# Performance work log

Hardware: AMD Instinct MI355X
Metric: run time of the kernel (lower is better)

Reference implementation:

```python
import jax, jax.numpy as jnp
import numpy as np

HEADS = 16
LN_EPS = 1e-5


def setup_inputs() -> dict:
    key = jax.random.key(0)
    ks = jax.random.split(key, 8)
    B, S, D = 2, 2048, 1024
    F = 4 * D
    std = 0.02
    return {
        "x": jax.random.normal(ks[0], (B, S, D), jnp.float32),
        # QKV projections (stored as (in, out)); kaiming-normal-like scale
        "Wq": jax.random.normal(ks[1], (D, D), jnp.float32) * std,
        "bq": jnp.zeros((D,), jnp.float32),
        "Wk": jax.random.normal(ks[2], (D, D), jnp.float32) * std,
        "bk": jnp.zeros((D,), jnp.float32),
        "Wv": jax.random.normal(ks[3], (D, D), jnp.float32) * std,
        "bv": jnp.zeros((D,), jnp.float32),
        # FFN
        "W1": jax.random.normal(ks[4], (D, F), jnp.float32) * std,
        "b1": jnp.zeros((F,), jnp.float32),
        "W2": jax.random.normal(ks[5], (F, D), jnp.float32) * std,
        "b2": jnp.zeros((D,), jnp.float32),
        # LayerNorm
        "gamma": jnp.ones((D,), jnp.float32),
        "beta": jnp.zeros((D,), jnp.float32),
    }


def reference(x, Wq, bq, Wk, bk, Wv, bv, W1, b1, W2, b2, gamma, beta):
    B, S, D = x.shape
    H = HEADS
    hd = D // H
    # QKV projections -> [B, H, S, hd]
    Q = (x @ Wq + bq).reshape(B, S, H, hd).transpose(0, 2, 1, 3)
    K = (x @ Wk + bk).reshape(B, S, H, hd).transpose(0, 2, 1, 3)
    V = (x @ Wv + bv).reshape(B, S, H, hd).transpose(0, 2, 1, 3)
    # scores scaled by sqrt(embedding_dim), faithful to source (not head_dim)
    scores = jnp.einsum('bhqd,bhkd->bhqk', Q, K) / jnp.sqrt(jnp.asarray(D, x.dtype))
    attn = jax.nn.softmax(scores, axis=-1)
    # diagonal_training: zero the diagonal of the post-softmax attention matrix
    attn = attn * (1.0 - jnp.eye(S, dtype=attn.dtype))
    out = jnp.einsum('bhqk,bhkd->bhqd', attn, V)
    out = out.transpose(0, 2, 1, 3).reshape(B, S, D)
    # dropout is identity in eval mode
    h = jax.nn.gelu(out @ W1 + b1, approximate=False) @ W2 + b2
    # LayerNorm
    mu = jnp.mean(h, axis=-1, keepdims=True)
    var = jnp.var(h, axis=-1, keepdims=True)
    return (h - mu) * jax.lax.rsqrt(var + LN_EPS) * gamma + beta
```

## Files before the change

kernel.cpp:

```cpp
#include <hip/hip_runtime.h>

using bf16x8 = __attribute__((ext_vector_type(8))) short;
using f32x4  = __attribute__((ext_vector_type(4))) float;

__device__ __forceinline__ float b2f(ushort u) {
  union { unsigned int i; float f; } v; v.i = ((unsigned int)u) << 16; return v.f;
}
__device__ __forceinline__ ushort f2b(float f) {
  unsigned int x = __float_as_uint(f);
  unsigned int r = (x + 0x7FFFu + ((x >> 16) & 1u)) >> 16;
  return (ushort)r;
}

__device__ __forceinline__ void gld_lds16(const void* g, void* l) {
  __builtin_amdgcn_global_load_lds(
      (const __attribute__((address_space(1))) void*)g,
      (__attribute__((address_space(3))) void*)l, 16, 0, 0);
}


__global__ void cast_bf16_kernel(const float* __restrict__ in, ushort* __restrict__ out, int n) {
  int i = (blockIdx.x * blockDim.x + threadIdx.x) * 4;
  if (i < n) {
    float4 v = *(const float4*)(in + i);
    ushort4 o = make_ushort4(f2b(v.x), f2b(v.y), f2b(v.z), f2b(v.w));
    *(ushort4*)(out + i) = o;
  }
}

__global__ void transpose_cast_kernel(const float* __restrict__ in, ushort* __restrict__ out,
                                      int R, int C) {
  __shared__ float tile[32][33];
  int tx = threadIdx.x, ty = threadIdx.y;
  int cb = blockIdx.x * 32, rb = blockIdx.y * 32;
  for (int i = ty; i < 32; i += 8)
    tile[i][tx] = in[(size_t)(rb + i) * C + (cb + tx)];
  __syncthreads();
  for (int i = ty; i < 32; i += 8)
    out[(size_t)(cb + i) * R + (rb + tx)] = f2b(tile[tx][i]);
}

__global__ void transpose_v_kernel(const ushort* __restrict__ V, ushort* __restrict__ Vt) {
  __shared__ ushort t[32][33];
  int bh = blockIdx.z;
  int s0 = blockIdx.x * 32, d0 = blockIdx.y * 32;
  const ushort* Vb = V + (size_t)bh * 2048 * 64;
  ushort* Vtb = Vt + (size_t)bh * 64 * 2048;
  int tx = threadIdx.x, ty = threadIdx.y;
  for (int i = ty; i < 32; i += 8) t[i][tx] = Vb[(size_t)(s0 + i) * 64 + d0 + tx];
  __syncthreads();
  for (int i = ty; i < 32; i += 8) Vtb[(size_t)(d0 + i) * 2048 + s0 + tx] = t[tx][i];
}


#define BM 128
#define BN 128
#define BK 32

template<int EPI>
__global__ __launch_bounds__(256) void gemm_bf16(
    const ushort* __restrict__ A, const ushort* __restrict__ Bt,
    const float* __restrict__ bias, void* __restrict__ Cout, void* __restrict__ Cout2,
    int M, int N, int Kstride, int k_len)
{
  __shared__ ushort Asm_[2][BM * BK];
  __shared__ ushort Bsm_[2][BN * BK];
  const int bm = blockIdx.x * BM, bn = blockIdx.y * BN;
  const int k_begin = blockIdx.z * k_len;
  const int tid = threadIdx.x;
  const int lane = tid & 63, w = tid >> 6;
  const int wm = (w >> 1) * 64, wn = (w & 1) * 64;
  const int g = lane >> 4, c = lane & 15;
  const int srow = tid >> 2, scol = (tid & 3) * 8;
  const int soff = srow * 32 + scol;

  const ushort* gA0 = A  + (size_t)(bm + srow) * Kstride + k_begin + scol;
  const ushort* gA1 = gA0 + (size_t)64 * Kstride;
  const ushort* gB0 = Bt + (size_t)(bn + srow) * Kstride + k_begin + scol;
  const ushort* gB1 = gB0 + (size_t)64 * Kstride;

  f32x4 acc[4][4] = {};
  const int nt = k_len / BK;

  gld_lds16(gA0, &Asm_[0][soff]);
  gld_lds16(gA1, &Asm_[0][64 * 32 + soff]);
  gld_lds16(gB0, &Bsm_[0][soff]);
  gld_lds16(gB1, &Bsm_[0][64 * 32 + soff]);
  __syncthreads();

  int cur = 0;
  for (int t = 0; t < nt; ++t) {
    if (t + 1 < nt) {
      int k0 = (t + 1) * BK;
      gld_lds16(gA0 + k0, &Asm_[cur ^ 1][soff]);
      gld_lds16(gA1 + k0, &Asm_[cur ^ 1][64 * 32 + soff]);
      gld_lds16(gB0 + k0, &Bsm_[cur ^ 1][soff]);
      gld_lds16(gB1 + k0, &Bsm_[cur ^ 1][64 * 32 + soff]);
    }
    bf16x8 af[4], bfr[4];
    #pragma unroll
    for (int m = 0; m < 4; ++m)
      af[m] = *(const bf16x8*)&Asm_[cur][(wm + m * 16 + c) * 32 + g * 8];
    #pragma unroll
    for (int n = 0; n < 4; ++n)
      bfr[n] = *(const bf16x8*)&Bsm_[cur][(wn + n * 16 + c) * 32 + g * 8];
    #pragma unroll
    for (int m = 0; m < 4; ++m)
      #pragma unroll
      for (int n = 0; n < 4; ++n)
        acc[m][n] = __builtin_amdgcn_mfma_f32_16x16x32_bf16(af[m], bfr[n], acc[m][n], 0, 0, 0);
    __syncthreads();
    cur ^= 1;
  }

  #pragma unroll
  for (int n = 0; n < 4; ++n) {
    int col = bn + wn + n * 16 + c;
    float bia = bias ? bias[col] : 0.0f;
    #pragma unroll
    for (int m = 0; m < 4; ++m) {
      #pragma unroll
      for (int r = 0; r < 4; ++r) {
        int row = bm + wm + m * 16 + g * 4 + r;
        float v = acc[m][n][r] + bia;
        if (EPI == 1) {
          float u = 0.7978845608028654f * (v + 0.044715f * v * v * v);
          float au = fabsf(u);
          float e = __expf(-2.0f * au);
          float th = (1.0f - e) / (1.0f + e);
          th = copysignf(th, u);
          v = 0.5f * v * (1.0f + th);
        }
        if (EPI == 2) {
          float* dst = (blockIdx.z == 0) ? (float*)Cout : (float*)Cout2;
          dst[(size_t)row * N + col] = v;
        } else if (EPI == 3) {
          int b = row >> 11, s = row & 2047;
          int which = col >> 10, cc = col & 1023;
          int hh = cc >> 6, d = cc & 63;
          ((ushort*)Cout)[(size_t)which * 4194304 +
                          ((size_t)((b * 16 + hh) * 2048 + s)) * 64 + d] = f2b(v);
        } else {
          ((ushort*)Cout)[(size_t)row * N + col] = f2b(v);
        }
      }
    }
  }
}


#define ATT_SC 0.03125f

__global__ __launch_bounds__(256) void attn_kernel(
    const ushort* __restrict__ Q, const ushort* __restrict__ K,
    const ushort* __restrict__ V, const ushort* __restrict__ Vt,
    ushort* __restrict__ Out)
{
  const int bh = blockIdx.y;
  const int b = bh >> 4, h = bh & 15;
  const int q0 = blockIdx.x * 64;
  const int tid = threadIdx.x;
  const int w = tid >> 6, lane = tid & 63;
  const int hi = lane >> 4, c = lane & 15;
  const int qw = q0 + w * 16;

  const ushort* Qb = Q + (size_t)bh * 2048 * 64;
  const ushort* Kb = K + (size_t)bh * 2048 * 64;
  const ushort* Vb = V + (size_t)bh * 2048 * 64;
  const ushort* Vtb = Vt + (size_t)bh * 64 * 2048;

  __shared__ ushort Ksm[64 * 72];
  __shared__ ushort Vsm[64 * 72];
  __shared__ ushort Psm[4][16 * 72];

  bf16x8 qf0 = *(const bf16x8*)(Qb + (size_t)(qw + c) * 64 + hi * 8);
  bf16x8 qf1 = *(const bf16x8*)(Qb + (size_t)(qw + c) * 64 + 32 + hi * 8);

  f32x4 acc[4] = {};
  float m_run = -1e30f, l_run = 0.f;

  const int srow = tid >> 2;
  const int scol = (tid & 3) * 8;

  for (int j0 = 0; j0 < 2048; j0 += 64) {
    __syncthreads();
    *(int4*)&Ksm[srow * 72 + scol]      = *(const int4*)(Kb + (size_t)(j0 + srow) * 64 + scol);
    *(int4*)&Ksm[srow * 72 + 32 + scol] = *(const int4*)(Kb + (size_t)(j0 + srow) * 64 + 32 + scol);
    *(int4*)&Vsm[srow * 72 + scol]      = *(const int4*)(Vtb + (size_t)srow * 2048 + j0 + scol);
    *(int4*)&Vsm[srow * 72 + 32 + scol] = *(const int4*)(Vtb + (size_t)srow * 2048 + j0 + 32 + scol);
    __syncthreads();

    f32x4 sv[4];
    #pragma unroll
    for (int sub = 0; sub < 4; ++sub) {
      bf16x8 k0 = *(const bf16x8*)&Ksm[(sub * 16 + c) * 72 + hi * 8];
      bf16x8 k1 = *(const bf16x8*)&Ksm[(sub * 16 + c) * 72 + 32 + hi * 8];
      f32x4 z = {};
      z = __builtin_amdgcn_mfma_f32_16x16x32_bf16(k0, qf0, z, 0, 0, 0);
      z = __builtin_amdgcn_mfma_f32_16x16x32_bf16(k1, qf1, z, 0, 0, 0);
      #pragma unroll
      for (int r = 0; r < 4; ++r) sv[sub][r] = z[r] * ATT_SC;
    }

    float tm = -1e30f;
    #pragma unroll
    for (int sub = 0; sub < 4; ++sub)
      #pragma unroll
      for (int r = 0; r < 4; ++r) tm = fmaxf(tm, sv[sub][r]);
    tm = fmaxf(tm, __shfl_xor(tm, 16));
    tm = fmaxf(tm, __shfl_xor(tm, 32));
    float mnew = fmaxf(m_run, tm);
    float p[16];
    float psum = 0.f;
    #pragma unroll
    for (int sub = 0; sub < 4; ++sub)
      #pragma unroll
      for (int r = 0; r < 4; ++r) { float e = __expf(sv[sub][r] - mnew); p[sub * 4 + r] = e; psum += e; }
    psum += __shfl_xor(psum, 16);
    psum += __shfl_xor(psum, 32);
    float f = __expf(m_run - mnew);
    l_run = l_run * f + psum;
    m_run = mnew;

    #pragma unroll
    for (int r = 0; r < 4; ++r) {
      float fr = __shfl(f, hi * 4 + r, 16);
      #pragma unroll
      for (int dsub = 0; dsub < 4; ++dsub) acc[dsub][r] *= fr;
    }

    #pragma unroll
    for (int sub = 0; sub < 4; ++sub) {
      ushort4 pk = make_ushort4(f2b(p[sub * 4 + 0]), f2b(p[sub * 4 + 1]),
                                f2b(p[sub * 4 + 2]), f2b(p[sub * 4 + 3]));
      *(ushort4*)&Psm[w][c * 72 + sub * 16 + hi * 4] = pk;
    }
    asm volatile("" ::: "memory");

    bf16x8 pa0 = *(const bf16x8*)&Psm[w][c * 72 + hi * 8];
    bf16x8 pa1 = *(const bf16x8*)&Psm[w][c * 72 + 32 + hi * 8];
    #pragma unroll
    for (int dsub = 0; dsub < 4; ++dsub) {
      bf16x8 v0 = *(const bf16x8*)&Vsm[(dsub * 16 + c) * 72 + hi * 8];
      bf16x8 v1 = *(const bf16x8*)&Vsm[(dsub * 16 + c) * 72 + 32 + hi * 8];
      acc[dsub] = __builtin_amdgcn_mfma_f32_16x16x32_bf16(pa0, v0, acc[dsub], 0, 0, 0);
      acc[dsub] = __builtin_amdgcn_mfma_f32_16x16x32_bf16(pa1, v1, acc[dsub], 0, 0, 0);
    }
  }

  #pragma unroll
  for (int r = 0; r < 4; ++r) {
    int q = qw + hi * 4 + r;
    float part = 0.f;
    #pragma unroll
    for (int t = 0; t < 4; ++t)
      part += b2f(Qb[(size_t)q * 64 + c * 4 + t]) * b2f(Kb[(size_t)q * 64 + c * 4 + t]);
    #pragma unroll
    for (int off = 1; off < 16; off <<= 1) part += __shfl_xor(part, off);
    float mq = __shfl(m_run, hi * 4 + r, 16);
    float lq = __shfl(l_run, hi * 4 + r, 16);
    float pqq = __expf(part * ATT_SC - mq);
    float inv = 1.f / lq;
    #pragma unroll
    for (int dsub = 0; dsub < 4; ++dsub) {
      float vq = b2f(Vb[(size_t)q * 64 + dsub * 16 + c]);
      float o = (acc[dsub][r] - pqq * vq) * inv;
      Out[((size_t)(b * 2048 + q) * 16 + h) * 64 + dsub * 16 + c] = f2b(o);
    }
  }
}


__global__ __launch_bounds__(256) void ln_kernel(float* __restrict__ h,
                                                 const float* __restrict__ p1,
                                                 const float* __restrict__ b2,
                                                 const float* __restrict__ gamma,
                                                 const float* __restrict__ beta) {
  int row = blockIdx.x, tid = threadIdx.x;
  float* hr = h + (size_t)row * 1024;
  const float* pr = p1 + (size_t)row * 1024;
  float4 v = ((const float4*)hr)[tid];
  float4 p = ((const float4*)pr)[tid];
  float4 bb = ((const float4*)b2)[tid];
  v.x += p.x + bb.x; v.y += p.y + bb.y; v.z += p.z + bb.z; v.w += p.w + bb.w;
  float s = v.x + v.y + v.z + v.w;
  #pragma unroll
  for (int off = 1; off < 64; off <<= 1) s += __shfl_xor(s, off);
  __shared__ float red[2][4];
  int wv = tid >> 6, lane = tid & 63;
  if (lane == 0) red[0][wv] = s;
  __syncthreads();
  float mu = (red[0][0] + red[0][1] + red[0][2] + red[0][3]) * (1.0f / 1024.0f);
  float dx = v.x - mu, dy = v.y - mu, dz = v.z - mu, dw = v.w - mu;
  float q = dx * dx + dy * dy + dz * dz + dw * dw;
  #pragma unroll
  for (int off = 1; off < 64; off <<= 1) q += __shfl_xor(q, off);
  if (lane == 0) red[1][wv] = q;
  __syncthreads();
  float var = (red[1][0] + red[1][1] + red[1][2] + red[1][3]) * (1.0f / 1024.0f);
  float is = rsqrtf(var + 1e-5f);
  float4 gm = ((const float4*)gamma)[tid];
  float4 bt = ((const float4*)beta)[tid];
  float4 o;
  o.x = dx * is * gm.x + bt.x;
  o.y = dy * is * gm.y + bt.y;
  o.z = dz * is * gm.z + bt.z;
  o.w = dw * is * gm.w + bt.w;
  ((float4*)hr)[tid] = o;
}


extern "C" void kernel_launch(void* const* d_in, const int* in_sizes, int n_in,
                              void* d_out, int out_size, void* d_ws, size_t ws_size,
                              hipStream_t stream) {
  const float* x  = (const float*)d_in[0];
  const float* Wq = (const float*)d_in[1];
  const float* bq = (const float*)d_in[2];
  const float* Wk = (const float*)d_in[3];
  const float* bk = (const float*)d_in[4];
  const float* Wv = (const float*)d_in[5];
  const float* bv = (const float*)d_in[6];
  const float* W1 = (const float*)d_in[7];
  const float* b1 = (const float*)d_in[8];
  const float* W2 = (const float*)d_in[9];
  const float* b2 = (const float*)d_in[10];
  const float* gamma = (const float*)d_in[11];
  const float* beta  = (const float*)d_in[12];
  float* out = (float*)d_out;

  char* ws = (char*)d_ws;
  const size_t MB = 1u << 20;
  ushort* xb    = (ushort*)(ws + 0);
  ushort* Wqkvt = (ushort*)(ws + 8 * MB);
  ushort* Qb    = (ushort*)(ws + 14 * MB);
  ushort* Kb    = (ushort*)(ws + 22 * MB);
  ushort* Vb    = (ushort*)(ws + 30 * MB);
  ushort* Vt    = (ushort*)(ws + 38 * MB);
  ushort* AO    = (ushort*)(ws + 46 * MB);
  ushort* W1t   = (ushort*)(ws + 0);
  ushort* h1    = (ushort*)(ws + 14 * MB);
  ushort* W2t   = (ushort*)(ws + 46 * MB);
  float*  p1    = (float*)(ws + 0);
  float*  bqkv  = (float*)(ws + 61 * MB);

  (void)hipMemcpyAsync(bqkv,        bq, 4096, hipMemcpyDeviceToDevice, stream);
  (void)hipMemcpyAsync(bqkv + 1024, bk, 4096, hipMemcpyDeviceToDevice, stream);
  (void)hipMemcpyAsync(bqkv + 2048, bv, 4096, hipMemcpyDeviceToDevice, stream);

  dim3 tb(32, 8);
  cast_bf16_kernel<<<4096, 256, 0, stream>>>(x, xb, 4194304);
  transpose_cast_kernel<<<dim3(32, 32), tb, 0, stream>>>(Wq, Wqkvt, 1024, 1024);
  transpose_cast_kernel<<<dim3(32, 32), tb, 0, stream>>>(Wk, Wqkvt + 1024 * 1024, 1024, 1024);
  transpose_cast_kernel<<<dim3(32, 32), tb, 0, stream>>>(Wv, Wqkvt + 2 * 1024 * 1024, 1024, 1024);

  gemm_bf16<3><<<dim3(32, 24), 256, 0, stream>>>(xb, Wqkvt, bqkv, Qb, nullptr,
                                                 4096, 3072, 1024, 1024);

  transpose_cast_kernel<<<dim3(128, 32), tb, 0, stream>>>(W1, W1t, 1024, 4096);
  transpose_v_kernel<<<dim3(64, 2, 32), tb, 0, stream>>>(Vb, Vt);

  attn_kernel<<<dim3(32, 32), 256, 0, stream>>>(Qb, Kb, Vb, Vt, AO);

  gemm_bf16<1><<<dim3(32, 32), 256, 0, stream>>>(AO, W1t, b1, h1, nullptr,
                                                 4096, 4096, 1024, 1024);
  transpose_cast_kernel<<<dim3(32, 128), tb, 0, stream>>>(W2, W2t, 4096, 1024);
  gemm_bf16<2><<<dim3(32, 8, 2), 256, 0, stream>>>(h1, W2t, nullptr, out, p1,
                                                   4096, 1024, 4096, 2048);

  ln_kernel<<<4096, 256, 0, stream>>>(out, p1, b2, gamma, beta);
}
```

Measured before the change: 282.0 us.

## Double-buffer attention K/V tiles via direct-to-LDS loads with swizzle and 512-thread blocks

```diff
diff --git a/kernel.cpp b/kernel.cpp
--- a/kernel.cpp
+++ b/kernel.cpp
@@ -10,6 +10,11 @@
   unsigned int x = __float_as_uint(f);
   unsigned int r = (x + 0x7FFFu + ((x >> 16) & 1u)) >> 16;
   return (ushort)r;
+}
+__device__ __forceinline__ unsigned cvt_pk_bf16(float a, float b) {
+  unsigned r;
+  asm("v_cvt_pk_bf16_f32 %0, %1, %2" : "=v"(r) : "v"(a), "v"(b));
+  return r;
 }
 
 __device__ __forceinline__ void gld_lds16(const void* g, void* l) {
@@ -149,16 +154,16 @@
 }
 
 
-#define ATT_SC 0.03125f
-
-__global__ __launch_bounds__(256) void attn_kernel(
+#define ATT_SC2 0.0450842202f
+
+__global__ __launch_bounds__(512) void attn_kernel(
     const ushort* __restrict__ Q, const ushort* __restrict__ K,
     const ushort* __restrict__ V, const ushort* __restrict__ Vt,
     ushort* __restrict__ Out)
 {
   const int bh = blockIdx.y;
   const int b = bh >> 4, h = bh & 15;
-  const int q0 = blockIdx.x * 64;
+  const int q0 = blockIdx.x * 128;
   const int tid = threadIdx.x;
   const int w = tid >> 6, lane = tid & 63;
   const int hi = lane >> 4, c = lane & 15;
@@ -169,9 +174,15 @@
   const ushort* Vb = V + (size_t)bh * 2048 * 64;
   const ushort* Vtb = Vt + (size_t)bh * 64 * 2048;
 
-  __shared__ ushort Ksm[64 * 72];
-  __shared__ ushort Vsm[64 * 72];
-  __shared__ ushort Psm[4][16 * 72];
+  __shared__ ushort Ksm[2][64 * 64];
+  __shared__ ushort Vsm[2][64 * 64];
+  __shared__ ushort Psm[8][16 * 72];
+
+  const int srow = tid >> 3;
+  const int sslot = tid & 7;
+  const int scolx = ((sslot ^ (srow & 7)) * 8);
+  const ushort* gK = Kb + (size_t)srow * 64 + scolx;
+  const ushort* gV = Vtb + (size_t)srow * 2048 + scolx;
 
   bf16x8 qf0 = *(const bf16x8*)(Qb + (size_t)(qw + c) * 64 + hi * 8);
   bf16x8 qf1 = *(const bf16x8*)(Qb + (size_t)(qw + c) * 64 + 32 + hi * 8);
@@ -179,27 +190,32 @@
   f32x4 acc[4] = {};
   float m_run = -1e30f, l_run = 0.f;
 
-  const int srow = tid >> 2;
-  const int scol = (tid & 3) * 8;
-
-  for (int j0 = 0; j0 < 2048; j0 += 64) {
-    __syncthreads();
-    *(int4*)&Ksm[srow * 72 + scol]      = *(const int4*)(Kb + (size_t)(j0 + srow) * 64 + scol);
-    *(int4*)&Ksm[srow * 72 + 32 + scol] = *(const int4*)(Kb + (size_t)(j0 + srow) * 64 + 32 + scol);
-    *(int4*)&Vsm[srow * 72 + scol]      = *(const int4*)(Vtb + (size_t)srow * 2048 + j0 + scol);
-    *(int4*)&Vsm[srow * 72 + 32 + scol] = *(const int4*)(Vtb + (size_t)srow * 2048 + j0 + 32 + scol);
-    __syncthreads();
+  gld_lds16(gK, &Ksm[0][tid * 8]);
+  gld_lds16(gV, &Vsm[0][tid * 8]);
+  __syncthreads();
+
+  const int nt = 2048 / 64;
+  for (int t = 0; t < nt; ++t) {
+    const int buf = t & 1;
+    if (t + 1 < nt) {
+      gld_lds16(gK + (size_t)(t + 1) * 64 * 64, &Ksm[buf ^ 1][tid * 8]);
+      gld_lds16(gV + (size_t)(t + 1) * 64,      &Vsm[buf ^ 1][tid * 8]);
+    }
 
     f32x4 sv[4];
     #pragma unroll
     for (int sub = 0; sub < 4; ++sub) {
-      bf16x8 k0 = *(const bf16x8*)&Ksm[(sub * 16 + c) * 72 + hi * 8];
-      bf16x8 k1 = *(const bf16x8*)&Ksm[(sub * 16 + c) * 72 + 32 + hi * 8];
+      int rr = sub * 16 + c;
+      int sw = (rr & 7) * 8;
+      bf16x8 k0 = *(const bf16x8*)&Ksm[buf][rr * 64 + ((hi * 8) ^ sw)];
+      bf16x8 k1 = *(const bf16x8*)&Ksm[buf][rr * 64 + ((32 + hi * 8) ^ sw)];
       f32x4 z = {};
+      __builtin_amdgcn_s_setprio(1);
       z = __builtin_amdgcn_mfma_f32_16x16x32_bf16(k0, qf0, z, 0, 0, 0);
       z = __builtin_amdgcn_mfma_f32_16x16x32_bf16(k1, qf1, z, 0, 0, 0);
-      #pragma unroll
-      for (int r = 0; r < 4; ++r) sv[sub][r] = z[r] * ATT_SC;
+      __builtin_amdgcn_s_setprio(0);
+      #pragma unroll
+      for (int r = 0; r < 4; ++r) sv[sub][r] = z[r] * ATT_SC2;
     }
 
     float tm = -1e30f;
@@ -215,10 +231,10 @@
     #pragma unroll
     for (int sub = 0; sub < 4; ++sub)
       #pragma unroll
-      for (int r = 0; r < 4; ++r) { float e = __expf(sv[sub][r] - mnew); p[sub * 4 + r] = e; psum += e; }
+      for (int r = 0; r < 4; ++r) { float e = exp2f(sv[sub][r] - mnew); p[sub * 4 + r] = e; psum += e; }
     psum += __shfl_xor(psum, 16);
     psum += __shfl_xor(psum, 32);
-    float f = __expf(m_run - mnew);
+    float f = exp2f(m_run - mnew);
     l_run = l_run * f + psum;
     m_run = mnew;
 
@@ -231,21 +247,28 @@
 
     #pragma unroll
     for (int sub = 0; sub < 4; ++sub) {
-      ushort4 pk = make_ushort4(f2b(p[sub * 4 + 0]), f2b(p[sub * 4 + 1]),
-                                f2b(p[sub * 4 + 2]), f2b(p[sub * 4 + 3]));
-      *(ushort4*)&Psm[w][c * 72 + sub * 16 + hi * 4] = pk;
+      uint2 pk;
+      pk.x = cvt_pk_bf16(p[sub * 4 + 0], p[sub * 4 + 1]);
+      pk.y = cvt_pk_bf16(p[sub * 4 + 2], p[sub * 4 + 3]);
+      *(uint2*)&Psm[w][c * 72 + sub * 16 + hi * 4] = pk;
     }
     asm volatile("" ::: "memory");
 
     bf16x8 pa0 = *(const bf16x8*)&Psm[w][c * 72 + hi * 8];
     bf16x8 pa1 = *(const bf16x8*)&Psm[w][c * 72 + 32 + hi * 8];
+    __builtin_amdgcn_s_setprio(1);
     #pragma unroll
     for (int dsub = 0; dsub < 4; ++dsub) {
-      bf16x8 v0 = *(const bf16x8*)&Vsm[(dsub * 16 + c) * 72 + hi * 8];
-      bf16x8 v1 = *(const bf16x8*)&Vsm[(dsub * 16 + c) * 72 + 32 + hi * 8];
+      int rr = dsub * 16 + c;
+      int sw = (rr & 7) * 8;
+      bf16x8 v0 = *(const bf16x8*)&Vsm[buf][rr * 64 + ((hi * 8) ^ sw)];
+      bf16x8 v1 = *(const bf16x8*)&Vsm[buf][rr * 64 + ((32 + hi * 8) ^ sw)];
       acc[dsub] = __builtin_amdgcn_mfma_f32_16x16x32_bf16(pa0, v0, acc[dsub], 0, 0, 0);
       acc[dsub] = __builtin_amdgcn_mfma_f32_16x16x32_bf16(pa1, v1, acc[dsub], 0, 0, 0);
     }
+    __builtin_amdgcn_s_setprio(0);
+
+    __syncthreads();
   }
 
   #pragma unroll
@@ -259,7 +282,7 @@
     for (int off = 1; off < 16; off <<= 1) part += __shfl_xor(part, off);
     float mq = __shfl(m_run, hi * 4 + r, 16);
     float lq = __shfl(l_run, hi * 4 + r, 16);
-    float pqq = __expf(part * ATT_SC - mq);
+    float pqq = exp2f(part * ATT_SC2 - mq);
     float inv = 1.f / lq;
     #pragma unroll
     for (int dsub = 0; dsub < 4; ++dsub) {
@@ -359,7 +382,7 @@
   transpose_cast_kernel<<<dim3(128, 32), tb, 0, stream>>>(W1, W1t, 1024, 4096);
   transpose_v_kernel<<<dim3(64, 2, 32), tb, 0, stream>>>(Vb, Vt);
 
-  attn_kernel<<<dim3(32, 32), 256, 0, stream>>>(Qb, Kb, Vb, Vt, AO);
+  attn_kernel<<<dim3(16, 32), 512, 0, stream>>>(Qb, Kb, Vb, Vt, AO);
 
   gemm_bf16<1><<<dim3(32, 32), 256, 0, stream>>>(AO, W1t, b1, h1, nullptr,
                                                  4096, 4096, 1024, 1024);
```

Result: faster. 270.5 us (-4.1%).
